# Kernel optimization log

Measured on AMD Instinct MI355X. Metric: run time of the kernel, lower is better.

Reference implementation:

```python
import jax, jax.numpy as jnp
import numpy as np

N, E = 50000, 800000
NFEAT, NHID, NHEADS, NCLASS = 512, 64, 8, 64
ALPHA = 0.2  # leaky relu negative slope


def setup_inputs() -> dict:
    key = jax.random.key(0)
    ks = jax.random.split(key, 8)
    x = jax.random.normal(ks[0], (N, NFEAT), jnp.float32)
    row = jax.random.randint(ks[1], (E,), 0, N)  # destination node i of each edge
    col = jax.random.randint(ks[2], (E,), 0, N)  # source node j of each edge
    W = jax.random.normal(ks[3], (NHEADS, NFEAT, NHID), jnp.float32) * (1.0 / np.sqrt(NFEAT))
    a = jax.random.normal(ks[4], (NHEADS, 2 * NHID), jnp.float32) * 0.1
    W_out = jax.random.normal(ks[5], (NHID * NHEADS, NCLASS), jnp.float32) * (1.0 / np.sqrt(NHID * NHEADS))
    a_out = jax.random.normal(ks[6], (2 * NCLASS,), jnp.float32) * 0.1
    return {"x": x, "row": row, "col": col, "W": W, "a": a, "W_out": W_out, "a_out": a_out}


def _gat_layer(h, W, a, row, col, n, alpha, concat):
    # h: [N, F_in], W: [F_in, F'], a: [2*F']
    Wh = h @ W                                   # [N, F']
    f = Wh.shape[-1]
    f_dst = Wh @ a[:f]                           # a^T part for target node i, [N]
    f_src = Wh @ a[f:]                           # a^T part for source node j, [N]
    e = jax.nn.leaky_relu(f_dst[row] + f_src[col], alpha)       # [E] attention logits
    # numerically stable segment softmax over incoming edges of each node
    m = jax.ops.segment_max(e, row, num_segments=n)
    m = jnp.where(jnp.isneginf(m), 0.0, m)       # nodes with no in-edges
    p = jnp.exp(e - m[row])
    denom = jax.ops.segment_sum(p, row, num_segments=n)
    att = p / jnp.maximum(denom[row], 1e-16)     # [E]
    out = jax.ops.segment_sum(att[:, None] * Wh[col], row, num_segments=n)  # [N, F']
    return jax.nn.elu(out) if concat else out


def reference(x, row, col, W, a, W_out, a_out):
    # eval mode: F.dropout is a no-op
    heads = [_gat_layer(x, W[h], a[h], row, col, N, ALPHA, True) for h in range(NHEADS)]
    h = jnp.concatenate(heads, axis=1)           # [N, NHID*NHEADS]
    return _gat_layer(h, W_out, a_out, row, col, N, ALPHA, False)  # [N, NCLASS]
```

## Files before the change

kernel.cpp:

```cpp
#include <hip/hip_runtime.h>
#include <cstdint>
#include <cstddef>

#define NN      50000
#define MPAD    50048
#define EE      800000
#define NHEADS  8
#define HID_TOT 512
#define NCLASS  64
#define ALPHA_LRELU 0.2f
#define NB1     196
#define GM1_M   391
#define GM1_B   (GM1_M * 4)

typedef unsigned short u16;
typedef __attribute__((ext_vector_type(8))) unsigned short ushort8;
typedef __attribute__((ext_vector_type(4))) unsigned short ushort4v;

__device__ __forceinline__ float bf2f(u16 v) {
    return __uint_as_float(((unsigned)v) << 16);
}
__device__ __forceinline__ u16 f2bf(float f) {
    unsigned u = __float_as_uint(f);
    return (u16)((u + 0x7fffu + ((u >> 16) & 1u)) >> 16);
}

#define PREP_R0 (MPAD * 64)
#define PREP_R1 (512 * 512)
#define PREP_R2 (64 * 512)
#define PREP_TOT (PREP_R0 + PREP_R1 + PREP_R2 + EE)

__global__ __launch_bounds__(256) void prep_all(const float* __restrict__ x,
                                                const float* __restrict__ W,
                                                const float* __restrict__ W_out,
                                                u16* __restrict__ xb,
                                                u16* __restrict__ Wt1,
                                                u16* __restrict__ Wto,
                                                const int* __restrict__ row,
                                                int* __restrict__ cnt) {
    int g = blockIdx.x * 256 + threadIdx.x;
    if (g < PREP_R0) {
        int r = g >> 6;
        int c = (g & 63) * 8;
        ushort8 o = (ushort8)0;
        if (r < NN) {
            const float4 v0 = *(const float4*)(x + (size_t)r * 512 + c);
            const float4 v1 = *(const float4*)(x + (size_t)r * 512 + c + 4);
            o[0] = f2bf(v0.x); o[1] = f2bf(v0.y); o[2] = f2bf(v0.z); o[3] = f2bf(v0.w);
            o[4] = f2bf(v1.x); o[5] = f2bf(v1.y); o[6] = f2bf(v1.z); o[7] = f2bf(v1.w);
        }
        *(ushort8*)(xb + (size_t)r * 512 + c) = o;
        return;
    }
    g -= PREP_R0;
    if (g < PREP_R1) {
        int c = g >> 9, f = g & 511;
        int h = c >> 6, j = c & 63;
        Wt1[g] = f2bf(W[(h << 15) + (f << 6) + j]);
        return;
    }
    g -= PREP_R1;
    if (g < PREP_R2) {
        int n = g >> 9, k = g & 511;
        Wto[g] = f2bf(W_out[k * 64 + n]);
        return;
    }
    g -= PREP_R2;
    if (g < EE) {
        atomicAdd(&cnt[row[g]], 1);
    }
}


__global__ __launch_bounds__(256) void scan_blocksum(const int* __restrict__ cnt,
                                                     int* __restrict__ bsum) {
    int idx = blockIdx.x * 256 + threadIdx.x;
    int v = (idx < NN) ? cnt[idx] : 0;
    #pragma unroll
    for (int o = 32; o; o >>= 1) v += __shfl_xor(v, o);
    __shared__ int sw[4];
    int wave = threadIdx.x >> 6;
    if ((threadIdx.x & 63) == 0) sw[wave] = v;
    __syncthreads();
    if (threadIdx.x == 0) bsum[blockIdx.x] = sw[0] + sw[1] + sw[2] + sw[3];
}

__global__ __launch_bounds__(256) void scan_write(const int* __restrict__ cnt,
                                                  const int* __restrict__ bsum,
                                                  int* __restrict__ start,
                                                  int* __restrict__ wr) {
    __shared__ int sh[256];
    __shared__ int swb[4];
    int t = threadIdx.x;
    int vb = (t < NB1 && t < blockIdx.x) ? bsum[t] : 0;
    #pragma unroll
    for (int o = 32; o; o >>= 1) vb += __shfl_xor(vb, o);
    if ((t & 63) == 0) swb[t >> 6] = vb;
    __syncthreads();
    const int blockoff = swb[0] + swb[1] + swb[2] + swb[3];

    int idx = blockIdx.x * 256 + t;
    int c = (idx < NN) ? cnt[idx] : 0;
    __syncthreads();
    sh[t] = c;
    __syncthreads();
    for (int o = 1; o < 256; o <<= 1) {
        int cur = sh[t];
        int add = (t >= o) ? sh[t - o] : 0;
        __syncthreads();
        sh[t] = cur + add;
        __syncthreads();
    }
    if (idx < NN) {
        int excl = blockoff + sh[t] - c;
        start[idx] = excl;
        wr[idx] = excl;
    }
    if (idx == 0) start[NN] = EE;
}


__device__ __forceinline__ void load_lds_128(const u16* g, u16* l) {
    __builtin_amdgcn_global_load_lds((const __attribute__((address_space(1))) void*)g,
                                     (__attribute__((address_space(3))) void*)l,
                                     16, 0, 0);
}

typedef __attribute__((ext_vector_type(8))) short frag8;
typedef __attribute__((ext_vector_type(4))) float f32x4;

__global__ __launch_bounds__(256) void scat_gemm1(const int* __restrict__ row,
                                                  const int* __restrict__ col,
                                                  int* __restrict__ wr,
                                                  int* __restrict__ ecol,
                                                  const u16* __restrict__ A,
                                                  const u16* __restrict__ Bt,
                                                  u16* __restrict__ C,
                                                  const float* __restrict__ av,
                                                  float* __restrict__ fd,
                                                  float* __restrict__ fs) {
    constexpr int BM = 128, BN = 128, BK = 32, WN = 64, NT = 4;
    constexpr int M = NN, N = 512, K = 512;
    __shared__ u16 As[BM * BK];
    __shared__ u16 Bs[BN * BK];
    const int tid = threadIdx.x;
    const int bid = blockIdx.x;

    const int e0 = (bid * 256 + tid) * 2;
    int sc0 = 0, sc1 = 0, sp0 = 0, sp1 = 0;
    bool edo = (e0 < EE);
    if (edo) {
        int2 rr = *(const int2*)(row + e0);
        int2 cc = *(const int2*)(col + e0);
        sc0 = cc.x; sc1 = cc.y;
        sp0 = atomicAdd(&wr[rr.x], 1);
        sp1 = atomicAdd(&wr[rr.y], 1);
    }

    const int wave = tid >> 6, lane = tid & 63;
    const int wm = wave & 1, wn = wave >> 1;
    const int bm = (bid % GM1_M) * BM;
    const int bnb = bid / GM1_M;
    const int bn = bnb * BN;
    const int q = lane >> 4, lr = lane & 15;

    f32x4 acc[4][NT] = {};

    for (int k0 = 0; k0 < K; k0 += BK) {
        #pragma unroll
        for (int c = wave; c < (BM * BK) / 512; c += 4) {
            int f = c * 512 + lane * 8;
            int r_ = f >> 5, ck = f & 31;
            load_lds_128(A + (size_t)(bm + r_) * K + k0 + ck, As + c * 512);
        }
        #pragma unroll
        for (int c = wave; c < (BN * BK) / 512; c += 4) {
            int f = c * 512 + lane * 8;
            int r_ = f >> 5, ck = f & 31;
            load_lds_128(Bt + (size_t)(bn + r_) * K + k0 + ck, Bs + c * 512);
        }
        __syncthreads();
        frag8 af[4], bfr[NT];
        #pragma unroll
        for (int am = 0; am < 4; am++)
            af[am] = *(const frag8*)(As + (wm * 64 + am * 16 + lr) * 32 + q * 8);
        #pragma unroll
        for (int bt = 0; bt < NT; bt++)
            bfr[bt] = *(const frag8*)(Bs + (wn * WN + bt * 16 + lr) * 32 + q * 8);
        #pragma unroll
        for (int am = 0; am < 4; am++)
            #pragma unroll
            for (int bt = 0; bt < NT; bt++)
                acc[am][bt] = __builtin_amdgcn_mfma_f32_16x16x32_bf16(af[am], bfr[bt], acc[am][bt], 0, 0, 0);
        __syncthreads();
    }

    if (edo) {
        ecol[sp0] = sc0;
        ecol[sp1] = sc1;
    }

    const int hd = bnb * 2 + wn;
    const float* ah = av + hd * 128;
    float adv[NT], adv2[NT];
    #pragma unroll
    for (int bt = 0; bt < NT; bt++) {
        adv[bt]  = ah[bt * 16 + lr];
        adv2[bt] = ah[64 + bt * 16 + lr];
    }

    #pragma unroll
    for (int am = 0; am < 4; am++) {
        #pragma unroll
        for (int reg = 0; reg < 4; reg++) {
            int gr = bm + wm * 64 + am * 16 + q * 4 + reg;
            bool inb = gr < M;
            if (inb) {
                #pragma unroll
                for (int bt = 0; bt < NT; bt++) {
                    int gc = bn + wn * WN + bt * 16 + lr;
                    C[(size_t)gr * N + gc] = f2bf(acc[am][bt][reg]);
                }
            }
            float sd = 0.f, ss = 0.f;
            #pragma unroll
            for (int bt = 0; bt < NT; bt++) {
                float v = acc[am][bt][reg];
                sd += v * adv[bt];
                ss += v * adv2[bt];
            }
            #pragma unroll
            for (int o = 1; o < 16; o <<= 1) {
                sd += __shfl_xor(sd, o);
                ss += __shfl_xor(ss, o);
            }
            if (lr == 0 && inb) {
                fd[gr * 8 + hd] = sd;
                fs[gr * 8 + hd] = ss;
            }
        }
    }
}

template <int BN, int OUT_MODE, int FUSE>
__global__ __launch_bounds__(256) void gemm_bf16(const u16* __restrict__ A,
                                                 const u16* __restrict__ Bt,
                                                 void* __restrict__ Cv,
                                                 int M, int N, int K,
                                                 const float* __restrict__ av,
                                                 float* __restrict__ fd,
                                                 float* __restrict__ fs) {
    constexpr int BM = 128, BK = 32;
    constexpr int WN = BN / 2;
    constexpr int NT = WN / 16;
    __shared__ u16 As[BM * BK];
    __shared__ u16 Bs[BN * BK];
    __shared__ float pd[2][2][64];
    __shared__ float ps[2][2][64];
    const int tid = threadIdx.x;
    const int wave = tid >> 6, lane = tid & 63;
    const int wm = wave & 1, wn = wave >> 1;
    const int bm = blockIdx.x * BM, bn = blockIdx.y * BN;
    const int q = lane >> 4, lr = lane & 15;

    f32x4 acc[4][NT] = {};

    for (int k0 = 0; k0 < K; k0 += BK) {
        #pragma unroll
        for (int c = wave; c < (BM * BK) / 512; c += 4) {
            int f = c * 512 + lane * 8;
            int row = f >> 5, ck = f & 31;
            load_lds_128(A + (size_t)(bm + row) * K + k0 + ck, As + c * 512);
        }
        #pragma unroll
        for (int c = wave; c < (BN * BK) / 512; c += 4) {
            int f = c * 512 + lane * 8;
            int row = f >> 5, ck = f & 31;
            load_lds_128(Bt + (size_t)(bn + row) * K + k0 + ck, Bs + c * 512);
        }
        __syncthreads();
        frag8 af[4], bfr[NT];
        #pragma unroll
        for (int am = 0; am < 4; am++)
            af[am] = *(const frag8*)(As + (wm * 64 + am * 16 + lr) * 32 + q * 8);
        #pragma unroll
        for (int bt = 0; bt < NT; bt++)
            bfr[bt] = *(const frag8*)(Bs + (wn * WN + bt * 16 + lr) * 32 + q * 8);
        #pragma unroll
        for (int am = 0; am < 4; am++)
            #pragma unroll
            for (int bt = 0; bt < NT; bt++)
                acc[am][bt] = __builtin_amdgcn_mfma_f32_16x16x32_bf16(af[am], bfr[bt], acc[am][bt], 0, 0, 0);
        __syncthreads();
    }

    float adv[NT], adv2[NT];
    int hd = 0;
    if (FUSE == 1) {
        hd = blockIdx.y * 2 + wn;
        const float* ah = av + hd * 128;
        #pragma unroll
        for (int bt = 0; bt < NT; bt++) {
            adv[bt]  = ah[bt * 16 + lr];
            adv2[bt] = ah[64 + bt * 16 + lr];
        }
    }
    if (FUSE == 2) {
        #pragma unroll
        for (int bt = 0; bt < NT; bt++) {
            adv[bt]  = av[wn * WN + bt * 16 + lr];
            adv2[bt] = av[64 + wn * WN + bt * 16 + lr];
        }
    }

    #pragma unroll
    for (int am = 0; am < 4; am++) {
        #pragma unroll
        for (int reg = 0; reg < 4; reg++) {
            int gr = bm + wm * 64 + am * 16 + q * 4 + reg;
            bool inb = gr < M;
            if (inb) {
                #pragma unroll
                for (int bt = 0; bt < NT; bt++) {
                    int gc = bn + wn * WN + bt * 16 + lr;
                    float v = acc[am][bt][reg];
                    if (OUT_MODE == 0) ((float*)Cv)[(size_t)gr * N + gc] = v;
                    else               ((u16*)Cv)[(size_t)gr * N + gc] = f2bf(v);
                }
            }
            if (FUSE != 0) {
                float sd = 0.f, ss = 0.f;
                #pragma unroll
                for (int bt = 0; bt < NT; bt++) {
                    float v = acc[am][bt][reg];
                    sd += v * adv[bt];
                    ss += v * adv2[bt];
                }
                #pragma unroll
                for (int o = 1; o < 16; o <<= 1) {
                    sd += __shfl_xor(sd, o);
                    ss += __shfl_xor(ss, o);
                }
                if (FUSE == 1) {
                    if (lr == 0 && inb) {
                        fd[gr * 8 + hd] = sd;
                        fs[gr * 8 + hd] = ss;
                    }
                } else {
                    if (lr == 0) {
                        int rr = am * 16 + q * 4 + reg;
                        pd[wm][wn][rr] = sd;
                        ps[wm][wn][rr] = ss;
                    }
                }
            }
        }
    }
    if (FUSE == 2) {
        __syncthreads();
        if (tid < 128) {
            int wmm = tid >> 6, rr = tid & 63;
            int gr = bm + wmm * 64 + rr;
            if (gr < M) {
                fd[gr] = pd[wmm][0][rr] + pd[wmm][1][rr];
                fs[gr] = ps[wmm][0][rr] + ps[wmm][1][rr];
            }
        }
    }
}

__global__ __launch_bounds__(256) void agg1_fused(const int* __restrict__ start,
                                                  const int* __restrict__ ecol,
                                                  const float* __restrict__ fd,
                                                  const float* __restrict__ fs,
                                                  const u16* __restrict__ Whb,
                                                  u16* __restrict__ h1b) {
    const int i = blockIdx.x * 4 + (threadIdx.x >> 6);
    const int lane = threadIdx.x & 63;
    const int hh = lane >> 3;
    const int st = start[i], en = start[i + 1];
    const float fdv = fd[i * 8 + hh];

    float acc[8] = {};
    float den = 0.f;
    int t = st;
    for (; t + 2 <= en; t += 2) {
        int j0 = ecol[t], j1 = ecol[t + 1];
        float v0 = fdv + fs[j0 * 8 + hh]; v0 = v0 > 0.f ? v0 : ALPHA_LRELU * v0;
        float v1 = fdv + fs[j1 * 8 + hh]; v1 = v1 > 0.f ? v1 : ALPHA_LRELU * v1;
        float p0 = __expf(v0);
        float p1 = __expf(v1);
        ushort8 w0 = *(const ushort8*)(Whb + (size_t)j0 * HID_TOT + lane * 8);
        ushort8 w1 = *(const ushort8*)(Whb + (size_t)j1 * HID_TOT + lane * 8);
        den += p0 + p1;
        #pragma unroll
        for (int k = 0; k < 8; k++) acc[k] += p0 * bf2f(w0[k]);
        #pragma unroll
        for (int k = 0; k < 8; k++) acc[k] += p1 * bf2f(w1[k]);
    }
    if (t < en) {
        int j = ecol[t];
        float v = fdv + fs[j * 8 + hh]; v = v > 0.f ? v : ALPHA_LRELU * v;
        float p = __expf(v);
        den += p;
        ushort8 wv = *(const ushort8*)(Whb + (size_t)j * HID_TOT + lane * 8);
        #pragma unroll
        for (int k = 0; k < 8; k++) acc[k] += p * bf2f(wv[k]);
    }
    float rden = 1.0f / fmaxf(den, 1e-16f);
    ushort8 o8;
    #pragma unroll
    for (int k = 0; k < 8; k++) {
        float v = acc[k] * rden;
        v = v > 0.f ? v : (__expf(v) - 1.0f);
        o8[k] = f2bf(v);
    }
    *(ushort8*)(h1b + (size_t)i * HID_TOT + lane * 8) = o8;
}

__global__ __launch_bounds__(256) void agg2_fused(const int* __restrict__ start,
                                                  const int* __restrict__ ecol,
                                                  const float* __restrict__ fd,
                                                  const float* __restrict__ fs,
                                                  const u16* __restrict__ Wh2b,
                                                  float* __restrict__ out) {
    const int i = blockIdx.x * 4 + (threadIdx.x >> 6);
    const int lane = threadIdx.x & 63;
    const int g = lane >> 4, r = lane & 15;
    const int st = start[i], en = start[i + 1];
    const float fdv = fd[i];

    float acc[4] = {};
    float den = 0.f;
    for (int t = st + g; t < en; t += 4) {
        int j = ecol[t];
        float v = fdv + fs[j];
        v = v > 0.f ? v : ALPHA_LRELU * v;
        float p = __expf(v);
        den += p;
        ushort4v wv = *(const ushort4v*)(Wh2b + (size_t)j * NCLASS + r * 4);
        #pragma unroll
        for (int k = 0; k < 4; k++) acc[k] += p * bf2f(wv[k]);
    }
    #pragma unroll
    for (int o = 16; o <= 32; o <<= 1) {
        den += __shfl_xor(den, o);
        #pragma unroll
        for (int k = 0; k < 4; k++) acc[k] += __shfl_xor(acc[k], o);
    }
    if (g == 0) {
        float rden = 1.0f / fmaxf(den, 1e-16f);
        float4 o4;
        o4.x = acc[0] * rden; o4.y = acc[1] * rden;
        o4.z = acc[2] * rden; o4.w = acc[3] * rden;
        *(float4*)(out + (size_t)i * NCLASS + r * 4) = o4;
    }
}


static inline int cdiv_l(long a, long b) { return (int)((a + b - 1) / b); }

extern "C" void kernel_launch(void* const* d_in, const int* in_sizes, int n_in,
                              void* d_out, int out_size, void* d_ws, size_t ws_size,
                              hipStream_t stream) {
    const float* x     = (const float*)d_in[0];
    const int*   row   = (const int*)d_in[1];
    const int*   col   = (const int*)d_in[2];
    const float* W     = (const float*)d_in[3];
    const float* a     = (const float*)d_in[4];
    const float* W_out = (const float*)d_in[5];
    const float* a_out = (const float*)d_in[6];
    float* out = (float*)d_out;

    char* wsb = (char*)d_ws;
    size_t off = 0;
    auto alloc = [&](size_t bytes) { char* p = wsb + off; off += (bytes + 255) & ~(size_t)255; return p; };
    u16*   xb     = (u16*)  alloc((size_t)MPAD * 512 * 2);
    u16*   Wcat_t = (u16*)  alloc((size_t)512 * 512 * 2);
    u16*   Wot_t  = (u16*)  alloc((size_t)64 * 512 * 2);
    u16*   Whb1   = (u16*)  alloc((size_t)NN * 512 * 2);
    float* fd1    = (float*)alloc((size_t)NN * 8 * 4);
    float* fs1    = (float*)alloc((size_t)NN * 8 * 4);
    u16*   h1b    = (u16*)  alloc((size_t)MPAD * 512 * 2);
    u16*   Wh2b   = (u16*)  alloc((size_t)NN * 64 * 2);
    float* fd2    = (float*)alloc((size_t)NN * 4);
    float* fs2    = (float*)alloc((size_t)NN * 4);
    int*   cnt    = (int*)  alloc((size_t)NN * 4);
    int*   startp = (int*)  alloc(((size_t)NN + 1) * 4);
    int*   wr     = (int*)  alloc((size_t)NN * 4);
    int*   ecol   = (int*)  alloc((size_t)EE * 4);
    int*   bsum   = (int*)  alloc((size_t)NB1 * 4);
    int*   boff   = (int*)  alloc((size_t)NB1 * 4);
    (void)boff;

    hipMemsetAsync(cnt, 0, (size_t)NN * 4, stream);
    prep_all<<<cdiv_l(PREP_TOT, 256), 256, 0, stream>>>(x, W, W_out, xb, Wcat_t, Wot_t,
                                                        row, cnt);

    scan_blocksum<<<NB1, 256, 0, stream>>>(cnt, bsum);
    scan_write<<<NB1, 256, 0, stream>>>(cnt, bsum, startp, wr);

    scat_gemm1<<<GM1_B, 256, 0, stream>>>(row, col, wr, ecol,
                                          xb, Wcat_t, Whb1, a, fd1, fs1);

    agg1_fused<<<NN / 4, 256, 0, stream>>>(startp, ecol, fd1, fs1, Whb1, h1b);

    {
        dim3 grid(cdiv_l(MPAD, 128), 1);
        gemm_bf16<64, 1, 2><<<grid, 256, 0, stream>>>(h1b, Wot_t, Wh2b, NN, 64, 512,
                                                      a_out, fd2, fs2);
    }
    agg2_fused<<<NN / 4, 256, 0, stream>>>(startp, ecol, fd2, fs2, Wh2b, out);
}
```

Measured before the change: 472.2 us.

## Double-buffer LDS tiles in both bf16 GEMM kernels to overlap loads with MFMA

Splits the shared-memory A/B tiles into two ping-pong buffers in both GEMM kernels. The next K-slice is issued into the idle buffer before the MFMA work on the current one. The goal is to hide global-to-LDS load latency behind the MFMA work and to drop one barrier per K step. In exchange, LDS use per block doubles, which may lower occupancy. The unrolled-by-two loop assumes an even number of K tiles.

```diff
diff --git a/kernel.cpp b/kernel.cpp
--- a/kernel.cpp
+++ b/kernel.cpp
@@ -140,9 +140,9 @@
                                                   float* __restrict__ fd,
                                                   float* __restrict__ fs) {
     constexpr int BM = 128, BN = 128, BK = 32, WN = 64, NT = 4;
-    constexpr int M = NN, N = 512, K = 512;
-    __shared__ u16 As[BM * BK];
-    __shared__ u16 Bs[BN * BK];
+    constexpr int M = NN, N = 512, K = 512, KT = K / BK;
+    __shared__ u16 As0[BM * BK], As1[BM * BK];
+    __shared__ u16 Bs0[BN * BK], Bs1[BN * BK];
     const int tid = threadIdx.x;
     const int bid = blockIdx.x;
 
@@ -166,33 +166,43 @@
 
     f32x4 acc[4][NT] = {};
 
-    for (int k0 = 0; k0 < K; k0 += BK) {
+    auto stage = [&](u16* as, u16* bs, int k0) {
         #pragma unroll
         for (int c = wave; c < (BM * BK) / 512; c += 4) {
             int f = c * 512 + lane * 8;
             int r_ = f >> 5, ck = f & 31;
-            load_lds_128(A + (size_t)(bm + r_) * K + k0 + ck, As + c * 512);
+            load_lds_128(A + (size_t)(bm + r_) * K + k0 + ck, as + c * 512);
         }
         #pragma unroll
         for (int c = wave; c < (BN * BK) / 512; c += 4) {
             int f = c * 512 + lane * 8;
             int r_ = f >> 5, ck = f & 31;
-            load_lds_128(Bt + (size_t)(bn + r_) * K + k0 + ck, Bs + c * 512);
-        }
-        __syncthreads();
+            load_lds_128(Bt + (size_t)(bn + r_) * K + k0 + ck, bs + c * 512);
+        }
+    };
+    auto compute = [&](const u16* as, const u16* bs) {
         frag8 af[4], bfr[NT];
         #pragma unroll
         for (int am = 0; am < 4; am++)
-            af[am] = *(const frag8*)(As + (wm * 64 + am * 16 + lr) * 32 + q * 8);
+            af[am] = *(const frag8*)(as + (wm * 64 + am * 16 + lr) * 32 + q * 8);
         #pragma unroll
         for (int bt = 0; bt < NT; bt++)
-            bfr[bt] = *(const frag8*)(Bs + (wn * WN + bt * 16 + lr) * 32 + q * 8);
+            bfr[bt] = *(const frag8*)(bs + (wn * WN + bt * 16 + lr) * 32 + q * 8);
         #pragma unroll
         for (int am = 0; am < 4; am++)
             #pragma unroll
             for (int bt = 0; bt < NT; bt++)
                 acc[am][bt] = __builtin_amdgcn_mfma_f32_16x16x32_bf16(af[am], bfr[bt], acc[am][bt], 0, 0, 0);
-        __syncthreads();
+    };
+
+    stage(As0, Bs0, 0);
+    for (int kt = 0; kt < KT; kt += 2) {
+        __syncthreads();
+        if (kt + 1 < KT) stage(As1, Bs1, (kt + 1) * BK);
+        compute(As0, Bs0);
+        __syncthreads();
+        if (kt + 2 < KT) stage(As0, Bs0, (kt + 2) * BK);
+        compute(As1, Bs1);
     }
 
     if (edo) {
@@ -253,8 +263,8 @@
     constexpr int BM = 128, BK = 32;
     constexpr int WN = BN / 2;
     constexpr int NT = WN / 16;
-    __shared__ u16 As[BM * BK];
-    __shared__ u16 Bs[BN * BK];
+    __shared__ u16 As0[BM * BK], As1[BM * BK];
+    __shared__ u16 Bs0[BN * BK], Bs1[BN * BK];
     __shared__ float pd[2][2][64];
     __shared__ float ps[2][2][64];
     const int tid = threadIdx.x;
@@ -265,33 +275,44 @@
 
     f32x4 acc[4][NT] = {};
 
-    for (int k0 = 0; k0 < K; k0 += BK) {
+    auto stage = [&](u16* as, u16* bs, int k0) {
         #pragma unroll
         for (int c = wave; c < (BM * BK) / 512; c += 4) {
             int f = c * 512 + lane * 8;
             int row = f >> 5, ck = f & 31;
-            load_lds_128(A + (size_t)(bm + row) * K + k0 + ck, As + c * 512);
+            load_lds_128(A + (size_t)(bm + row) * K + k0 + ck, as + c * 512);
         }
         #pragma unroll
         for (int c = wave; c < (BN * BK) / 512; c += 4) {
             int f = c * 512 + lane * 8;
             int row = f >> 5, ck = f & 31;
-            load_lds_128(Bt + (size_t)(bn + row) * K + k0 + ck, Bs + c * 512);
-        }
-        __syncthreads();
+            load_lds_128(Bt + (size_t)(bn + row) * K + k0 + ck, bs + c * 512);
+        }
+    };
+    auto compute = [&](const u16* as, const u16* bs) {
         frag8 af[4], bfr[NT];
         #pragma unroll
         for (int am = 0; am < 4; am++)
-            af[am] = *(const frag8*)(As + (wm * 64 + am * 16 + lr) * 32 + q * 8);
+            af[am] = *(const frag8*)(as + (wm * 64 + am * 16 + lr) * 32 + q * 8);
         #pragma unroll
         for (int bt = 0; bt < NT; bt++)
-            bfr[bt] = *(const frag8*)(Bs + (wn * WN + bt * 16 + lr) * 32 + q * 8);
+            bfr[bt] = *(const frag8*)(bs + (wn * WN + bt * 16 + lr) * 32 + q * 8);
         #pragma unroll
         for (int am = 0; am < 4; am++)
             #pragma unroll
             for (int bt = 0; bt < NT; bt++)
                 acc[am][bt] = __builtin_amdgcn_mfma_f32_16x16x32_bf16(af[am], bfr[bt], acc[am][bt], 0, 0, 0);
-        __syncthreads();
+    };
+
+    const int KT = K / BK;
+    stage(As0, Bs0, 0);
+    for (int kt = 0; kt < KT; kt += 2) {
+        __syncthreads();
+        if (kt + 1 < KT) stage(As1, Bs1, (kt + 1) * BK);
+        compute(As0, Bs0);
+        __syncthreads();
+        if (kt + 2 < KT) stage(As0, Bs0, (kt + 2) * BK);
+        compute(As1, Bs1);
     }
 
     float adv[NT], adv2[NT];
```

Result: no change. 468.9 us (-0.7%).
